# Performance work log

Hardware: AMD Instinct MI355X
Metric: run time of the kernel (lower is better)

## Reference

```python
import jax, jax.numpy as jnp
import numpy as np

EPS = 1e-6      # vector-neurons EPS
BN_EPS = 1e-5   # torch BatchNorm2d default eps
NEG_SLOPE = 0.2 # VNLeakyReLU default
K = 20


def knn_idx(xf, k):
    # xf: (B, D, N) flattened features; returns (B, N, k) indices of nearest neighbors
    inner = -2.0 * jnp.einsum('bdn,bdm->bnm', xf, xf)
    xx = jnp.sum(xf * xf, axis=1)  # (B, N)
    neg_dist = -xx[:, :, None] - inner - xx[:, None, :]  # (B, N, N)
    _, idx = jax.lax.top_k(neg_dist, k)
    return idx


def get_graph_feature(x, k):
    # x: (B, C, 3, N) -> (B, 2C, 3, N, k)
    B, C, _, N = x.shape
    xf = x.reshape(B, C * 3, N)
    idx = knn_idx(xf, k)                      # (B, N, k)
    pts = x.transpose(0, 3, 1, 2)             # (B, N, C, 3)
    nbrs = jax.vmap(lambda p, i: p[i])(pts, idx)  # (B, N, k, C, 3)
    ctr = pts[:, :, None, :, :]               # (B, N, 1, C, 3)
    feat = jnp.concatenate([nbrs - ctr, jnp.broadcast_to(ctr, nbrs.shape)], axis=3)  # (B,N,k,2C,3)
    return feat.transpose(0, 3, 4, 1, 2)      # (B, 2C, 3, N, k)


def vn_batchnorm(p, gamma, beta):
    # p: (B, O, 3, N, K); BatchNorm2d on the vector norms (training-mode batch stats)
    norm = jnp.sqrt(jnp.sum(p * p, axis=2)) + EPS  # (B, O, N, K)
    mean = jnp.mean(norm, axis=(0, 2, 3))
    var = jnp.var(norm, axis=(0, 2, 3))            # biased, matches torch BN normalization
    g = gamma[None, :, None, None]
    b = beta[None, :, None, None]
    norm_bn = g * (norm - mean[None, :, None, None]) / jnp.sqrt(var[None, :, None, None] + BN_EPS) + b
    return p / norm[:, :, None] * norm_bn[:, :, None]


def vn_leaky_relu(p, Wd):
    d = jnp.einsum('oc,bcdnk->bodnk', Wd, p)
    dot = jnp.sum(p * d, axis=2, keepdims=True)
    d_nsq = jnp.sum(d * d, axis=2, keepdims=True)
    proj = p - (dot / (d_nsq + EPS)) * d
    return NEG_SLOPE * p + (1.0 - NEG_SLOPE) * jnp.where(dot >= 0, p, proj)


def setup_inputs() -> dict:
    key = jax.random.key(0)
    k1, k2, k3 = jax.random.split(key, 3)
    B, C, N = 2, 32, 8192
    out_feat, in_feat = 64, 64  # in_feat = 2*C
    x = jax.random.normal(k1, (B, C, 3, N), dtype=jnp.float32)
    W1 = jax.random.normal(k2, (out_feat, in_feat), dtype=jnp.float32) * (1.0 / np.sqrt(in_feat))
    Wd = jax.random.normal(k3, (out_feat, out_feat), dtype=jnp.float32) * (1.0 / np.sqrt(out_feat))
    gamma = jnp.ones((out_feat,), dtype=jnp.float32)
    beta = jnp.zeros((out_feat,), dtype=jnp.float32)
    return {"x": x, "W1": W1, "Wd": Wd, "gamma": gamma, "beta": beta}


def reference(x, W1, Wd, gamma, beta):
    # VNDGCNN.forward: get_graph_feature -> VNLinearAndLeakyReLU -> mean_pool over k
    feat = get_graph_feature(x, K)                       # (B, 2C, 3, N, k)
    p = jnp.einsum('oc,bcdnk->bodnk', W1, feat)          # VNLinear
    p = vn_batchnorm(p, gamma, beta)                     # VNBatchNorm (dim=5)
    p = vn_leaky_relu(p, Wd)                             # VNLeakyReLU
    return jnp.mean(p, axis=-1)                          # mean_pool -> (B, O, 3, N)
```

## Files before the change

kernel.cpp:

```cpp
#include <hip/hip_runtime.h>
#include <math.h>

#define NPTS 8192
#define NB 2
#define FDIM 96
#define KNN 20
#define VN_EPS 1e-6f
#define VN_BN_EPS 1e-5f
#define NSAMP 768
#define PSLOT 12
#define NPAN 64
#define ROWSLOT (NPAN * PSLOT)
#define CAPS 12
#define OVCAP 64
#define TSLOT 3
#define NTILE 2080

typedef float f32x16 __attribute__((ext_vector_type(16)));
typedef _Float16 f16x8 __attribute__((ext_vector_type(8)));
typedef unsigned short u16x8 __attribute__((ext_vector_type(8)));
typedef unsigned long long u64x2 __attribute__((ext_vector_type(2)));

#define WAVESYNC()                                            \
    do {                                                      \
        asm volatile("s_waitcnt lgkmcnt(0)" ::: "memory");    \
        __builtin_amdgcn_wave_barrier();                      \
        asm volatile("" ::: "memory");                        \
    } while (0)

__device__ __forceinline__ unsigned orderable(float v) {
    unsigned u = __float_as_uint(v);
    return (u & 0x80000000u) ? ~u : (u | 0x80000000u);
}
__device__ __forceinline__ float unorderable(unsigned k) {
    unsigned u = (k & 0x80000000u) ? (k & 0x7fffffffu) : ~k;
    return __uint_as_float(u);
}

__global__ __launch_bounds__(256) void k_prep(const float* __restrict__ x,
                                              float* __restrict__ xx,
                                              unsigned short* __restrict__ xs) {
    int m = blockIdx.x * 256 + threadIdx.x;
    int b = m >> 13, n = m & 8191;
    const float* xf = x + (size_t)b * FDIM * NPTS;
    unsigned short* row = xs + (size_t)m * 192;
    float s = 0.f;
    for (int fc = 0; fc < 12; ++fc) {
        u16x8 hv, lv;
        #pragma unroll
        for (int j = 0; j < 8; ++j) {
            float vv = xf[(size_t)(fc * 8 + j) * NPTS + n];
            s += vv * vv;
            _Float16 h = (_Float16)vv;
            float hf = (float)h;
            _Float16 l = (_Float16)(vv - hf);
            union { _Float16 f; unsigned short u; } ch, cl;
            ch.f = h; cl.f = l;
            hv[j] = ch.u; lv[j] = cl.u;
        }
        *(u16x8*)(row + fc * 8) = hv;
        *(u16x8*)(row + 96 + fc * 8) = lv;
    }
    xx[m] = s;
}

__global__ __launch_bounds__(256, 3) void k_thr(const unsigned short* __restrict__ xs,
                                                const float* __restrict__ xx,
                                                float* __restrict__ minibuf) {
    __shared__ __align__(16) unsigned short Bsl[128][104];
    __shared__ float sxr[128];
    __shared__ float sxc[128];
    int t = threadIdx.x;
    int lane = t & 63, wid = t >> 6;
    int l31 = lane & 31, hi = lane >> 5;
    int row0 = blockIdx.x * 128;
    int b = row0 >> 13;
    int panel = blockIdx.y;
    int m0 = panel * 128;
    const unsigned short* xsb = xs + (size_t)b * NPTS * 192;
    int n0w = (row0 & 8191) + wid * 32;

    f16x8 af[6];
    const unsigned short* arow = xsb + (size_t)(n0w + l31) * 192 + hi * 8;
    #pragma unroll
    for (int ks = 0; ks < 6; ++ks) af[ks] = *(const f16x8*)(arow + ks * 16);

    if (t < 128) {
        sxr[t] = xx[row0 + t];
        sxc[t] = xx[(b << 13) + m0 + t];
    }

    f32x16 acc[4];
    #pragma unroll
    for (int ct = 0; ct < 4; ++ct)
        #pragma unroll
        for (int e = 0; e < 16; ++e) acc[ct][e] = 0.f;

    int sc2 = t >> 1, sh2 = t & 1;
    auto stageB = [&](int part) {
        const unsigned short* sb = xsb + (size_t)(m0 + sc2) * 192 + part * 96 + sh2 * 48;
        unsigned short* db = &Bsl[sc2][sh2 * 48];
        #pragma unroll
        for (int j = 0; j < 6; ++j) *(u16x8*)(db + j * 8) = *(const u16x8*)(sb + j * 8);
    };
    auto mmpass = [&]() {
        #pragma unroll
        for (int ks = 0; ks < 6; ++ks)
            #pragma unroll
            for (int ct = 0; ct < 4; ++ct) {
                f16x8 bf = *(const f16x8*)&Bsl[ct * 32 + l31][ks * 16 + hi * 8];
                acc[ct] = __builtin_amdgcn_mfma_f32_32x32x16_f16(af[ks], bf, acc[ct], 0, 0, 0);
            }
    };

    stageB(1);
    __syncthreads();
    mmpass();
    __syncthreads();
    stageB(0);
    __syncthreads();
    mmpass();
    #pragma unroll
    for (int ks = 0; ks < 6; ++ks) af[ks] = *(const f16x8*)(arow + 96 + ks * 16);
    mmpass();

    float xc[4];
    #pragma unroll
    for (int ct = 0; ct < 4; ++ct) xc[ct] = sxc[ct * 32 + l31];
    #pragma unroll
    for (int q = 0; q < 4; ++q)
        #pragma unroll
        for (int rr = 0; rr < 4; ++rr) {
            int rowin = wid * 32 + 4 * hi + 8 * q + rr;
            float xr = sxr[rowin];
            #pragma unroll
            for (int ct = 0; ct < 4; ++ct) {
                float valx = 2.f * acc[ct][q * 4 + rr] - xr - xc[ct];
                minibuf[(size_t)(row0 + rowin) * NSAMP + m0 + ct * 32 + l31] = valx;
            }
        }
}

__global__ __launch_bounds__(256) void k_thrsel(const float* __restrict__ minibuf,
                                                float* __restrict__ tauF) {
    int t = threadIdx.x;
    int lane = t & 63, w = t >> 6;
    int r = blockIdx.x * 4 + w;
    const float* mp = minibuf + (size_t)r * NSAMP;
    unsigned key[12];
    #pragma unroll
    for (int s = 0; s < 12; ++s) key[s] = orderable(mp[lane + s * 64]);
    unsigned lo = 0, hi = 0x10000u;
    for (int it = 0; it < 16; ++it) {
        unsigned mid = (lo + hi) >> 1;
        unsigned mkey = mid << 16;
        int c = 0;
        #pragma unroll
        for (int s = 0; s < 12; ++s) c += (key[s] >= mkey) ? 1 : 0;
        #pragma unroll
        for (int d = 1; d < 64; d <<= 1) c += __shfl_xor(c, d);
        if (c >= KNN) lo = mid; else hi = mid;
    }
    if (lane == 0) {
        tauF[r] = (lo > 0u) ? unorderable((lo - 1u) << 16) : -3.4e38f;
    }
}

__global__ __launch_bounds__(256, 3) void k_distf(const unsigned short* __restrict__ xs,
                                                  const float* __restrict__ xx,
                                                  const float* __restrict__ tauF,
                                                  unsigned* __restrict__ cnt2d,
                                                  unsigned long long* __restrict__ cand,
                                                  unsigned* __restrict__ ovcnt,
                                                  unsigned long long* __restrict__ ovbuf) {
    __shared__ __align__(16) unsigned short Bsl[128][104];
    __shared__ float sxr[128];
    __shared__ float sxc[128];
    __shared__ float stauR[128];
    __shared__ float stauC[128];
    __shared__ unsigned tcl[128][4];
    __shared__ __align__(16) unsigned long long tstage[128][PSLOT];
    int t = threadIdx.x;
    int lane = t & 63, wid = t >> 6;
    int l31 = lane & 31, hi = lane >> 5;

    int bx = blockIdx.x;
    int batch = (bx >= NTILE) ? 1 : 0;
    int ti = bx - batch * NTILE;
    int R = 0;
    while (ti >= 64 - R) { ti -= 64 - R; ++R; }
    int C = R + ti;
    bool offdiag = (R != C);
    int rowL0 = R * 128;
    int m0 = C * 128;
    int rowG0 = batch * 8192 + rowL0;
    int colG0 = batch * 8192 + m0;
    const unsigned short* xsb = xs + (size_t)batch * NPTS * 192;
    int n0w = rowL0 + wid * 32;

    f16x8 af[6];
    const unsigned short* arow = xsb + (size_t)(n0w + l31) * 192 + hi * 8;
    #pragma unroll
    for (int ks = 0; ks < 6; ++ks) af[ks] = *(const f16x8*)(arow + ks * 16);

    if (t < 128) {
        sxr[t] = xx[rowG0 + t];
        stauR[t] = tauF[rowG0 + t];
        sxc[t] = xx[colG0 + t];
        stauC[t] = tauF[colG0 + t];
    }

    f32x16 acc[4];
    #pragma unroll
    for (int ct = 0; ct < 4; ++ct)
        #pragma unroll
        for (int e = 0; e < 16; ++e) acc[ct][e] = 0.f;

    int sc2 = t >> 1, sh2 = t & 1;
    auto stageB = [&](int part) {
        const unsigned short* sb = xsb + (size_t)(m0 + sc2) * 192 + part * 96 + sh2 * 48;
        unsigned short* db = &Bsl[sc2][sh2 * 48];
        #pragma unroll
        for (int j = 0; j < 6; ++j) *(u16x8*)(db + j * 8) = *(const u16x8*)(sb + j * 8);
    };
    auto mmpass = [&]() {
        #pragma unroll
        for (int ks = 0; ks < 6; ++ks)
            #pragma unroll
            for (int ct = 0; ct < 4; ++ct) {
                f16x8 bf = *(const f16x8*)&Bsl[ct * 32 + l31][ks * 16 + hi * 8];
                acc[ct] = __builtin_amdgcn_mfma_f32_32x32x16_f16(af[ks], bf, acc[ct], 0, 0, 0);
            }
    };

    stageB(1);
    __syncthreads();
    mmpass();
    __syncthreads();
    stageB(0);
    __syncthreads();
    mmpass();
    #pragma unroll
    for (int ks = 0; ks < 6; ++ks) af[ks] = *(const f16x8*)(arow + 96 + ks * 16);
    mmpass();

    float xc[4], stC[4];
    #pragma unroll
    for (int ct = 0; ct < 4; ++ct) {
        xc[ct] = sxc[ct * 32 + l31];
        stC[ct] = stauC[ct * 32 + l31];
    }
    unsigned tq[4] = {0u, 0u, 0u, 0u};
    #pragma unroll
    for (int q = 0; q < 4; ++q)
        #pragma unroll
        for (int rr = 0; rr < 4; ++rr) {
            int rowin = wid * 32 + 4 * hi + 8 * q + rr;
            int grow = rowG0 + rowin;
            float xr = sxr[rowin];
            float tau = stauR[rowin];
            unsigned cnt_run = 0;
            size_t base = (size_t)grow * ROWSLOT + (size_t)C * PSLOT;
            #pragma unroll
            for (int ct = 0; ct < 4; ++ct) {
                float valx = 2.f * acc[ct][q * 4 + rr] - xr - xc[ct];
                bool p = (valx >= tau);
                unsigned long long bal = __ballot(p);
                unsigned hm = hi ? (unsigned)(bal >> 32) : (unsigned)bal;
                if (p) {
                    unsigned key = orderable(valx);
                    unsigned pos = cnt_run + (unsigned)__popc(hm & ((1u << l31) - 1u));
                    unsigned long long e = ((unsigned long long)key << 32)
                                         | (unsigned)(m0 + ct * 32 + l31);
                    if (pos < PSLOT) {
                        cand[base + pos] = e;
                    } else {
                        unsigned o = atomicAdd(&ovcnt[grow], 1u);
                        if (o < OVCAP) ovbuf[(size_t)grow * OVCAP + o] = e;
                    }
                }
                cnt_run += (unsigned)__popc(hm);
                if (offdiag) {
                    bool pt = (valx >= stC[ct]);
                    unsigned long long balT = __ballot(pt);
                    unsigned b0 = (unsigned)((balT >> l31) & 1ull);
                    unsigned b1 = (unsigned)((balT >> (l31 + 32)) & 1ull);
                    if (pt) {
                        unsigned pos = tq[ct] + (hi ? b0 : 0u);
                        unsigned keyt = orderable(valx);
                        unsigned long long et = ((unsigned long long)keyt << 32)
                                              | (unsigned)(rowL0 + rowin);
                        unsigned slot = (unsigned)wid * TSLOT + pos;
                        if (pos < TSLOT) {
                            tstage[ct * 32 + l31][slot] = et;
                        } else {
                            int cG = colG0 + ct * 32 + l31;
                            unsigned o = atomicAdd(&ovcnt[cG], 1u);
                            if (o < OVCAP) ovbuf[(size_t)cG * OVCAP + o] = et;
                        }
                    }
                    tq[ct] += b0 + b1;
                }
            }
            if (l31 == 0)
                cnt2d[(size_t)grow * NPAN + C] = (cnt_run < PSLOT) ? cnt_run : PSLOT;
        }
    if (offdiag) {
        #pragma unroll
        for (int ct = 0; ct < 4; ++ct) {
            unsigned tv = tq[ct];
            tcl[ct * 32 + l31][wid] = (tv < (unsigned)TSLOT) ? tv : (unsigned)TSLOT;
        }
        __syncthreads();
        if (t < 128) {
            unsigned pq = tcl[t][0] | (tcl[t][1] << 8) | (tcl[t][2] << 16) | (tcl[t][3] << 24);
            cnt2d[(size_t)(colG0 + t) * NPAN + R] = pq;
            size_t tb = (size_t)(colG0 + t) * ROWSLOT + (size_t)R * PSLOT;
            #pragma unroll
            for (int s = 0; s < PSLOT; s += 2)
                *(u64x2*)&cand[tb + s] = *(const u64x2*)&tstage[t][s];
        }
    }
}

__global__ __launch_bounds__(256) void k_mrg(const unsigned long long* __restrict__ cand,
                                             const unsigned* __restrict__ cnt2d,
                                             const unsigned* __restrict__ ovcnt,
                                             const unsigned long long* __restrict__ ovbuf,
                                             int* __restrict__ idxOut) {
    int t = threadIdx.x;
    int lane = t & 63, w = t >> 6;
    int r = blockIdx.x * 4 + w;
    int B = (r & 8191) >> 7;
    __shared__ unsigned scc[4][NPAN];
    scc[w][lane] = cnt2d[(size_t)r * NPAN + lane];
    WAVESYNC();
    const unsigned long long* cp = cand + (size_t)r * ROWSLOT;
    unsigned long long pk[CAPS + 1];
    #pragma unroll
    for (int s = 0; s < CAPS; ++s) {
        int slot = lane + 64 * s;
        int panel = slot / PSLOT;
        int within = slot - panel * PSLOT;
        unsigned cc = scc[w][panel];
        bool valid;
        if (panel >= B) {
            valid = within < (int)cc;
        } else {
            int wv = within / TSLOT;
            int ws = within - wv * TSLOT;
            valid = ws < (int)((cc >> (8 * wv)) & 255u);
        }
        pk[s] = valid ? cp[slot] : 0ull;
    }
    int ovn = (int)ovcnt[r]; if (ovn > OVCAP) ovn = OVCAP;
    pk[CAPS] = (lane < ovn) ? ovbuf[(size_t)r * OVCAP + lane] : 0ull;

    unsigned lo = 0, hi = 0x10000u;
    for (int it = 0; it < 16; ++it) {
        unsigned mid = (lo + hi) >> 1;
        unsigned mkey = mid << 16;
        int c = 0;
        #pragma unroll
        for (int s = 0; s <= CAPS; ++s) c += ((unsigned)(pk[s] >> 32) >= mkey) ? 1 : 0;
        #pragma unroll
        for (int d = 1; d < 64; d <<= 1) c += __shfl_xor(c, d);
        if (c >= KNN) lo = mid; else hi = mid;
    }
    unsigned thr = lo << 16;

    __shared__ unsigned long long sk[4][128];
    __shared__ int sn[4];
    if (lane == 0) sn[w] = 0;
    WAVESYNC();
    #pragma unroll
    for (int s = 0; s <= CAPS; ++s) {
        if ((unsigned)(pk[s] >> 32) >= thr) {
            int j = atomicAdd(&sn[w], 1);
            if (j < 128) sk[w][j] = pk[s];
        }
    }
    WAVESYNC();
    int nc = sn[w]; if (nc > 128) nc = 128;
    #pragma unroll
    for (int half = 0; half < 2; ++half) {
        int i = lane + half * 64;
        if (i < nc) {
            unsigned long long me = sk[w][i];
            unsigned km = (unsigned)(me >> 32), cm = (unsigned)me;
            int rank = 0;
            for (int j = 0; j < nc; ++j) {
                unsigned long long o = sk[w][j];
                unsigned ko = (unsigned)(o >> 32), co = (unsigned)o;
                rank += (ko > km || (ko == km && co < cm)) ? 1 : 0;
            }
            if (rank < KNN) idxOut[(size_t)r * KNN + rank] = (int)cm;
        }
    }
}

__global__ __launch_bounds__(256) void k_uv(const float* __restrict__ x,
                                            const float* __restrict__ W1,
                                            float* __restrict__ u,
                                            float* __restrict__ v) {
    __shared__ float sA[64 * 33];
    __shared__ float sV[64 * 33];
    __shared__ float sxf[FDIM * 16];
    int t = threadIdx.x;
    for (int i = t; i < 64 * 32; i += 256) {
        int o = i >> 5, c = i & 31;
        float a = W1[o * 64 + c];
        sA[o * 33 + c] = a;
        sV[o * 33 + c] = W1[o * 64 + 32 + c] - a;
    }
    int p0 = blockIdx.x * 16;
    int b = p0 >> 13, nb = p0 & 8191;
    const float* xf = x + (size_t)b * FDIM * NPTS;
    for (int i = t; i < FDIM * 16; i += 256) {
        int f = i >> 4, p = i & 15;
        sxf[f * 16 + p] = xf[(size_t)f * NPTS + nb + p];
    }
    __syncthreads();
    #pragma unroll
    for (int ii = 0; ii < 4; ++ii) {
        int it = t + 256 * ii;
        int o = it & 63, p = it >> 6;
        float u0 = 0.f, u1 = 0.f, u2 = 0.f, w0 = 0.f, w1 = 0.f, w2 = 0.f;
        #pragma unroll
        for (int c = 0; c < 32; ++c) {
            float a = sA[o * 33 + c];
            float wv = sV[o * 33 + c];
            float x0 = sxf[(c * 3 + 0) * 16 + p];
            float x1 = sxf[(c * 3 + 1) * 16 + p];
            float x2 = sxf[(c * 3 + 2) * 16 + p];
            u0 += a * x0;  u1 += a * x1;  u2 += a * x2;
            w0 += wv * x0; w1 += wv * x1; w2 += wv * x2;
        }
        size_t base = ((size_t)(p0 + p) * 64 + o) * 3;
        u[base] = u0; u[base + 1] = u1; u[base + 2] = u2;
        v[base] = w0; v[base + 1] = w1; v[base + 2] = w2;
    }
}

__global__ __launch_bounds__(256) void k_stats(const float* __restrict__ u,
                                               const float* __restrict__ v,
                                               const int* __restrict__ idx,
                                               float* __restrict__ partial) {
    int blk = blockIdx.x, t = threadIdx.x;
    int o = t & 63, sub = t >> 6;
    int p0 = blk * 8;
    __shared__ float svf[8 * 192];
    __shared__ int sjf[8 * KNN];
    for (int i = t; i < 8 * 192; i += 256) svf[i] = v[(size_t)p0 * 192 + i];
    for (int i = t; i < 8 * KNN; i += 256) sjf[i] = idx[(size_t)p0 * KNN + i];
    __syncthreads();
    float s1 = 0.f, s2 = 0.f;
    for (int p = 0; p < 8; ++p) {
        int gpt = p0 + p;
        size_t ubase = (size_t)(gpt >> 13) * NPTS * 192;
        const float* vp = &svf[p * 192 + o * 3];
        float v0 = vp[0], v1 = vp[1], v2 = vp[2];
        for (int kk = sub; kk < KNN; kk += 4) {
            int j = sjf[p * KNN + kk];
            const float* up = u + ubase + (size_t)j * 192 + o * 3;
            float q0 = up[0] + v0, q1 = up[1] + v1, q2 = up[2] + v2;
            float nrm = sqrtf(q0 * q0 + q1 * q1 + q2 * q2) + VN_EPS;
            s1 += nrm;
            s2 += nrm * nrm;
        }
    }
    __shared__ float r1[256], r2[256];
    r1[t] = s1; r2[t] = s2;
    __syncthreads();
    if (t < 64) {
        float a1 = r1[t] + r1[t + 64] + r1[t + 128] + r1[t + 192];
        float a2 = r2[t] + r2[t + 64] + r2[t + 128] + r2[t + 192];
        partial[(size_t)blk * 128 + t] = a1;
        partial[(size_t)blk * 128 + 64 + t] = a2;
    }
}

__global__ __launch_bounds__(256) void k_reduce(const float* __restrict__ partial,
                                                const float* __restrict__ gamma,
                                                const float* __restrict__ beta,
                                                float* __restrict__ gsbs) {
    int ch = blockIdx.x, t = threadIdx.x;
    float s1 = 0.f, s2 = 0.f;
    for (int i = t; i < 2048; i += 256) {
        s1 += partial[(size_t)i * 128 + ch];
        s2 += partial[(size_t)i * 128 + 64 + ch];
    }
    __shared__ float r1[256], r2[256];
    r1[t] = s1; r2[t] = s2;
    __syncthreads();
    for (int s = 128; s > 0; s >>= 1) {
        if (t < s) { r1[t] += r1[t + s]; r2[t] += r2[t + s]; }
        __syncthreads();
    }
    if (t == 0) {
        const float cnt2 = (float)(NB * NPTS * KNN);
        float mean = r1[0] / cnt2;
        float var = r2[0] / cnt2 - mean * mean;
        float inv = 1.0f / sqrtf(var + VN_BN_EPS);
        float g = gamma[ch] * inv;
        gsbs[ch] = g;
        gsbs[64 + ch] = beta[ch] - mean * g;
    }
}

__global__ __launch_bounds__(64) void k_final(const float* __restrict__ u,
                                              const float* __restrict__ v,
                                              const int* __restrict__ idx,
                                              const float* __restrict__ Wd,
                                              const float* __restrict__ gsbs,
                                              float* __restrict__ out) {
    int lane = threadIdx.x;
    int l31 = lane & 31, hi = lane >> 5;
    int gpt = blockIdx.x;
    int b = gpt >> 13, n = gpt & 8191;

    __shared__ __align__(16) unsigned short Qw[30 * 72];
    __shared__ __align__(16) float Dw[30 * 64];

    f16x8 Bf[2][4];
    #pragma unroll
    for (int ct = 0; ct < 2; ++ct)
        #pragma unroll
        for (int ks = 0; ks < 4; ++ks) {
            const float* wp = Wd + (size_t)(ct * 32 + l31) * 64 + ks * 16 + hi * 8;
            f16x8 f;
            #pragma unroll
            for (int jj = 0; jj < 8; ++jj) f[jj] = (_Float16)wp[jj];
            Bf[ct][ks] = f;
        }

    float gso = gsbs[lane], bso = gsbs[64 + lane];
    size_t vb = (size_t)gpt * 192 + lane * 3;
    float v0 = v[vb], v1 = v[vb + 1], v2 = v[vb + 2];
    const int* jrow = idx + (size_t)gpt * KNN;
    size_t ubase = (size_t)b * NPTS * 192;
    float a0 = 0.f, a1 = 0.f, a2 = 0.f;

    for (int h = 0; h < 2; ++h) {
        #pragma unroll
        for (int kl = 0; kl < 10; ++kl) {
            int j = jrow[h * 10 + kl];
            const float* up = u + ubase + (size_t)j * 192 + lane * 3;
            float q0 = up[0] + v0, q1 = up[1] + v1, q2 = up[2] + v2;
            float nrm = sqrtf(q0 * q0 + q1 * q1 + q2 * q2) + VN_EPS;
            float f = (gso * nrm + bso) / nrm;
            q0 *= f; q1 *= f; q2 *= f;
            union { _Float16 f16; unsigned short u16; } c0, c1, c2;
            c0.f16 = (_Float16)q0; c1.f16 = (_Float16)q1; c2.f16 = (_Float16)q2;
            Qw[(3 * kl + 0) * 72 + lane] = c0.u16;
            Qw[(3 * kl + 1) * 72 + lane] = c1.u16;
            Qw[(3 * kl + 2) * 72 + lane] = c2.u16;
        }
        WAVESYNC();
        f32x16 acc[2];
        #pragma unroll
        for (int ct = 0; ct < 2; ++ct)
            #pragma unroll
            for (int e = 0; e < 16; ++e) acc[ct][e] = 0.f;
        #pragma unroll
        for (int ks = 0; ks < 4; ++ks) {
            f16x8 af = *(const f16x8*)&Qw[l31 * 72 + ks * 16 + hi * 8];
            acc[0] = __builtin_amdgcn_mfma_f32_32x32x16_f16(af, Bf[0][ks], acc[0], 0, 0, 0);
            acc[1] = __builtin_amdgcn_mfma_f32_32x32x16_f16(af, Bf[1][ks], acc[1], 0, 0, 0);
        }
        #pragma unroll
        for (int ct = 0; ct < 2; ++ct)
            #pragma unroll
            for (int q = 0; q < 4; ++q)
                #pragma unroll
                for (int r = 0; r < 4; ++r) {
                    int row = 4 * hi + 8 * q + r;
                    if (row < 30) Dw[row * 64 + ct * 32 + l31] = acc[ct][q * 4 + r];
                }
        WAVESYNC();
        #pragma unroll
        for (int kl = 0; kl < 10; ++kl) {
            float qd[3], dd[3];
            #pragma unroll
            for (int d = 0; d < 3; ++d) {
                union { unsigned short u16; _Float16 f16; } rr;
                rr.u16 = Qw[(3 * kl + d) * 72 + lane];
                qd[d] = (float)rr.f16;
                dd[d] = Dw[(3 * kl + d) * 64 + lane];
            }
            float dot = qd[0] * dd[0] + qd[1] * dd[1] + qd[2] * dd[2];
            float dn = dd[0] * dd[0] + dd[1] * dd[1] + dd[2] * dd[2];
            float coef = (dot >= 0.f) ? 0.f : 0.8f * dot / (dn + VN_EPS);
            a0 += qd[0] - coef * dd[0];
            a1 += qd[1] - coef * dd[1];
            a2 += qd[2] - coef * dd[2];
        }
        WAVESYNC();
    }
    float s = 1.f / (float)KNN;
    size_t ob = ((size_t)(b * 64 + lane) * 3) * NPTS + n;
    out[ob] = a0 * s;
    out[ob + NPTS] = a1 * s;
    out[ob + 2 * NPTS] = a2 * s;
}

extern "C" void kernel_launch(void* const* d_in, const int* in_sizes, int n_in,
                              void* d_out, int out_size, void* d_ws, size_t ws_size,
                              hipStream_t stream) {
    const float* x = (const float*)d_in[0];
    const float* W1 = (const float*)d_in[1];
    const float* Wd = (const float*)d_in[2];
    const float* gamma = (const float*)d_in[3];
    const float* beta = (const float*)d_in[4];
    float* out = (float*)d_out;

    char* ws = (char*)d_ws;
    size_t off = 0;
    auto alloc = [&](size_t bytes) {
        void* p = ws + off;
        off = (off + bytes + 255) & ~(size_t)255;
        return p;
    };
    const int totalRows = NB * NPTS;
    float* xxp = (float*)alloc((size_t)totalRows * 4);
    int* idxp = (int*)alloc((size_t)totalRows * KNN * 4);
    float* up = (float*)alloc((size_t)totalRows * 192 * 4);
    float* vp = (float*)alloc((size_t)totalRows * 192 * 4);
    float* partial = (float*)alloc((size_t)2048 * 128 * 4);
    float* gsbs = (float*)alloc(512);
    unsigned short* xsp = (unsigned short*)alloc((size_t)totalRows * 192 * 2);
    float* tauFp = (float*)alloc((size_t)totalRows * 4);
    unsigned* cnt2d = (unsigned*)alloc((size_t)totalRows * NPAN * 4);
    unsigned* ovcnt = (unsigned*)alloc((size_t)totalRows * 4);
    unsigned long long* ovbuf = (unsigned long long*)alloc((size_t)totalRows * OVCAP * 8);
    void* region = alloc((size_t)totalRows * ROWSLOT * 8);
    float* minibuf = (float*)region;
    unsigned long long* cand = (unsigned long long*)region;

    hipMemsetAsync(ovcnt, 0, (size_t)totalRows * 4, stream);

    k_prep<<<totalRows / 256, 256, 0, stream>>>(x, xxp, xsp);

    k_thr<<<dim3(totalRows / 128, NSAMP / 128), 256, 0, stream>>>(xsp, xxp, minibuf);
    k_thrsel<<<totalRows / 4, 256, 0, stream>>>(minibuf, tauFp);
    k_distf<<<NB * NTILE, 256, 0, stream>>>(xsp, xxp, tauFp, cnt2d, cand, ovcnt, ovbuf);
    k_mrg<<<totalRows / 4, 256, 0, stream>>>(cand, cnt2d, ovcnt, ovbuf, idxp);

    k_uv<<<totalRows / 16, 256, 0, stream>>>(x, W1, up, vp);
    k_stats<<<totalRows / 8, 256, 0, stream>>>(up, vp, idxp, partial);
    k_reduce<<<64, 256, 0, stream>>>(partial, gamma, beta, gsbs);
    k_final<<<totalRows, 64, 0, stream>>>(up, vp, idxp, Wd, gsbs, out);
}
```

Before: 392.2 us.

## Stage candidate slots in zeroed LDS and drop per-panel count array

```diff
diff --git a/kernel.cpp b/kernel.cpp
--- a/kernel.cpp
+++ b/kernel.cpp
@@ -169,7 +169,6 @@
 __global__ __launch_bounds__(256, 3) void k_distf(const unsigned short* __restrict__ xs,
                                                   const float* __restrict__ xx,
                                                   const float* __restrict__ tauF,
-                                                  unsigned* __restrict__ cnt2d,
                                                   unsigned long long* __restrict__ cand,
                                                   unsigned* __restrict__ ovcnt,
                                                   unsigned long long* __restrict__ ovbuf) {
@@ -178,8 +177,6 @@
     __shared__ float sxc[128];
     __shared__ float stauR[128];
     __shared__ float stauC[128];
-    __shared__ unsigned tcl[128][4];
-    __shared__ __align__(16) unsigned long long tstage[128][PSLOT];
     int t = threadIdx.x;
     int lane = t & 63, wid = t >> 6;
     int l31 = lane & 31, hi = lane >> 5;
@@ -244,6 +241,14 @@
     for (int ks = 0; ks < 6; ++ks) af[ks] = *(const f16x8*)(arow + 96 + ks * 16);
     mmpass();
 
+    __syncthreads();
+    unsigned long long* stg = (unsigned long long*)&Bsl[0][0];
+    #pragma unroll
+    for (int z = 0; z < 12; ++z) stg[t * 12 + z] = 0ull;
+    __syncthreads();
+    unsigned long long* ostage = stg;
+    unsigned long long* tstage = stg + 128 * PSLOT;
+
     float xc[4], stC[4];
     #pragma unroll
     for (int ct = 0; ct < 4; ++ct) {
@@ -260,7 +265,6 @@
             float xr = sxr[rowin];
             float tau = stauR[rowin];
             unsigned cnt_run = 0;
-            size_t base = (size_t)grow * ROWSLOT + (size_t)C * PSLOT;
             #pragma unroll
             for (int ct = 0; ct < 4; ++ct) {
                 float valx = 2.f * acc[ct][q * 4 + rr] - xr - xc[ct];
@@ -273,7 +277,7 @@
                     unsigned long long e = ((unsigned long long)key << 32)
                                          | (unsigned)(m0 + ct * 32 + l31);
                     if (pos < PSLOT) {
-                        cand[base + pos] = e;
+                        ostage[rowin * PSLOT + pos] = e;
                     } else {
                         unsigned o = atomicAdd(&ovcnt[grow], 1u);
                         if (o < OVCAP) ovbuf[(size_t)grow * OVCAP + o] = e;
@@ -292,7 +296,7 @@
                                               | (unsigned)(rowL0 + rowin);
                         unsigned slot = (unsigned)wid * TSLOT + pos;
                         if (pos < TSLOT) {
-                            tstage[ct * 32 + l31][slot] = et;
+                            tstage[(ct * 32 + l31) * PSLOT + slot] = et;
                         } else {
                             int cG = colG0 + ct * 32 + l31;
                             unsigned o = atomicAdd(&ovcnt[cG], 1u);
@@ -302,57 +306,33 @@
                     tq[ct] += b0 + b1;
                 }
             }
-            if (l31 == 0)
-                cnt2d[(size_t)grow * NPAN + C] = (cnt_run < PSLOT) ? cnt_run : PSLOT;
-        }
-    if (offdiag) {
-        #pragma unroll
-        for (int ct = 0; ct < 4; ++ct) {
-            unsigned tv = tq[ct];
-            tcl[ct * 32 + l31][wid] = (tv < (unsigned)TSLOT) ? tv : (unsigned)TSLOT;
-        }
-        __syncthreads();
-        if (t < 128) {
-            unsigned pq = tcl[t][0] | (tcl[t][1] << 8) | (tcl[t][2] << 16) | (tcl[t][3] << 24);
-            cnt2d[(size_t)(colG0 + t) * NPAN + R] = pq;
+        }
+    __syncthreads();
+    if (t < 128) {
+        size_t ob = (size_t)(rowG0 + t) * ROWSLOT + (size_t)C * PSLOT;
+        #pragma unroll
+        for (int s = 0; s < PSLOT; s += 2)
+            *(u64x2*)&cand[ob + s] = *(const u64x2*)&ostage[t * PSLOT + s];
+        if (offdiag) {
             size_t tb = (size_t)(colG0 + t) * ROWSLOT + (size_t)R * PSLOT;
             #pragma unroll
             for (int s = 0; s < PSLOT; s += 2)
-                *(u64x2*)&cand[tb + s] = *(const u64x2*)&tstage[t][s];
+                *(u64x2*)&cand[tb + s] = *(const u64x2*)&tstage[t * PSLOT + s];
         }
     }
 }
 
 __global__ __launch_bounds__(256) void k_mrg(const unsigned long long* __restrict__ cand,
-                                             const unsigned* __restrict__ cnt2d,
                                              const unsigned* __restrict__ ovcnt,
                                              const unsigned long long* __restrict__ ovbuf,
                                              int* __restrict__ idxOut) {
     int t = threadIdx.x;
     int lane = t & 63, w = t >> 6;
     int r = blockIdx.x * 4 + w;
-    int B = (r & 8191) >> 7;
-    __shared__ unsigned scc[4][NPAN];
-    scc[w][lane] = cnt2d[(size_t)r * NPAN + lane];
-    WAVESYNC();
     const unsigned long long* cp = cand + (size_t)r * ROWSLOT;
     unsigned long long pk[CAPS + 1];
     #pragma unroll
-    for (int s = 0; s < CAPS; ++s) {
-        int slot = lane + 64 * s;
-        int panel = slot / PSLOT;
-        int within = slot - panel * PSLOT;
-        unsigned cc = scc[w][panel];
-        bool valid;
-        if (panel >= B) {
-            valid = within < (int)cc;
-        } else {
-            int wv = within / TSLOT;
-            int ws = within - wv * TSLOT;
-            valid = ws < (int)((cc >> (8 * wv)) & 255u);
-        }
-        pk[s] = valid ? cp[slot] : 0ull;
-    }
+    for (int s = 0; s < CAPS; ++s) pk[s] = cp[lane + 64 * s];
     int ovn = (int)ovcnt[r]; if (ovn > OVCAP) ovn = OVCAP;
     pk[CAPS] = (lane < ovn) ? ovbuf[(size_t)r * OVCAP + lane] : 0ull;
 
@@ -368,6 +348,7 @@
         if (c >= KNN) lo = mid; else hi = mid;
     }
     unsigned thr = lo << 16;
+    if (thr == 0u) thr = 1u;
 
     __shared__ unsigned long long sk[4][128];
     __shared__ int sn[4];
@@ -630,7 +611,6 @@
     float* gsbs = (float*)alloc(512);
     unsigned short* xsp = (unsigned short*)alloc((size_t)totalRows * 192 * 2);
     float* tauFp = (float*)alloc((size_t)totalRows * 4);
-    unsigned* cnt2d = (unsigned*)alloc((size_t)totalRows * NPAN * 4);
     unsigned* ovcnt = (unsigned*)alloc((size_t)totalRows * 4);
     unsigned long long* ovbuf = (unsigned long long*)alloc((size_t)totalRows * OVCAP * 8);
     void* region = alloc((size_t)totalRows * ROWSLOT * 8);
@@ -643,8 +623,8 @@
 
     k_thr<<<dim3(totalRows / 128, NSAMP / 128), 256, 0, stream>>>(xsp, xxp, minibuf);
     k_thrsel<<<totalRows / 4, 256, 0, stream>>>(minibuf, tauFp);
-    k_distf<<<NB * NTILE, 256, 0, stream>>>(xsp, xxp, tauFp, cnt2d, cand, ovcnt, ovbuf);
-    k_mrg<<<totalRows / 4, 256, 0, stream>>>(cand, cnt2d, ovcnt, ovbuf, idxp);
+    k_distf<<<NB * NTILE, 256, 0, stream>>>(xsp, xxp, tauFp, cand, ovcnt, ovbuf);
+    k_mrg<<<totalRows / 4, 256, 0, stream>>>(cand, ovcnt, ovbuf, idxp);
 
     k_uv<<<totalRows / 16, 256, 0, stream>>>(x, W1, up, vp);
     k_stats<<<totalRows / 8, 256, 0, stream>>>(up, vp, idxp, partial);
```

Result: no change. 387.7 us (-1.1%).
